# Kernel tuning notes

Measured on AMD Instinct MI355X. Metric: run time of the kernel, lower is better.

Reference implementation:

```python
import jax, jax.numpy as jnp
import numpy as np

K_TOP = 2  # n_experts_per_tok
W_SCALE = 0.02  # keep activations numerically tame


def setup_inputs() -> dict:
    key = jax.random.key(0)
    ks = jax.random.split(key, 8)
    D, F, E = 1024, 1024, 8
    B, T = 4, 2048
    x = jax.random.normal(ks[0], (B, T, D), dtype=jnp.float32)
    router_w = jax.random.normal(ks[1], (D, E), dtype=jnp.float32) * W_SCALE
    sg = jax.random.normal(ks[2], (D, F), dtype=jnp.float32) * W_SCALE
    su = jax.random.normal(ks[3], (D, F), dtype=jnp.float32) * W_SCALE
    sd = jax.random.normal(ks[4], (F, D), dtype=jnp.float32) * W_SCALE
    wg = jax.random.normal(ks[5], (E, D, F), dtype=jnp.float32) * W_SCALE
    wu = jax.random.normal(ks[6], (E, D, F), dtype=jnp.float32) * W_SCALE
    wd = jax.random.normal(ks[7], (E, F, D), dtype=jnp.float32) * W_SCALE
    return {"x": x, "router_w": router_w, "sg": sg, "su": su, "sd": sd,
            "wg": wg, "wu": wu, "wd": wd}


def reference(x, router_w, sg, su, sd, wg, wu, wd):
    B, T, D = x.shape
    E = wg.shape[0]
    flat = x.reshape(-1, D)                       # [N, D]
    N = flat.shape[0]

    # shared SwiGLU expert (n_shared_experts = 1)
    shared = (jax.nn.silu(flat @ sg) * (flat @ su)) @ sd  # [N, D]

    # top-k softmax router with renormalization
    probs = jax.nn.softmax(flat @ router_w, axis=-1)      # [N, E]
    topk_p, topk_i = jax.lax.top_k(probs, K_TOP)          # [N, K]
    topk_p = topk_p / (jnp.sum(topk_p, axis=-1, keepdims=True) + 1e-9)

    # dense combine weights: scatter renormalized probs into [N, E]
    cw = jnp.zeros((N, E), dtype=flat.dtype).at[
        jnp.arange(N)[:, None], topk_i].add(topk_p)

    # per-expert SwiGLU on all tokens, weighted combine (jit-friendly MoE form)
    h = jax.nn.silu(jnp.einsum('nd,edf->nef', flat, wg)) \
        * jnp.einsum('nd,edf->nef', flat, wu)             # [N, E, F]
    eo = jnp.einsum('nef,efd->ned', h, wd)                # [N, E, D]
    routed = jnp.einsum('ned,ne->nd', eo, cw)             # [N, D]

    return (shared + routed).reshape(B, T, D)
```

## Files before the change

### kernel.cpp

```cpp
#include <hip/hip_runtime.h>

#define N_TOK    8192
#define D_DIM    1024
#define F_DIM    1024
#define NESH     9
#define MAX_RTD  18432
#define MAX_ROWS 26624
#define BM 256
#define BN 128
#define BK 64
#define BN2 256

#define MO 16
#define MT 25

typedef float  f4    __attribute__((ext_vector_type(4)));
typedef float  f32x4 __attribute__((ext_vector_type(4)));
typedef short  s16x8 __attribute__((ext_vector_type(8)));
typedef unsigned short u16x8 __attribute__((ext_vector_type(8)));

static __device__ __forceinline__ unsigned short f2bf(float f) {
    union { float f; unsigned u; } v; v.f = f;
    unsigned r = v.u + 0x7FFFu + ((v.u >> 16) & 1u);
    return (unsigned short)(r >> 16);
}
static __device__ __forceinline__ float bf2f(unsigned short u) {
    union { unsigned u; float f; } v; v.u = ((unsigned)u) << 16; return v.f;
}

#define GLDS(gp, lp) __builtin_amdgcn_global_load_lds( \
    (const __attribute__((address_space(1))) void*)(gp), \
    (__attribute__((address_space(3))) void*)(lp), 16, 0, 0)

#define RSWZ(row, idx) ((idx) ^ (((row) & 7) << 3))

__global__ __launch_bounds__(256) void k_convert_x(
    const float* __restrict__ x, unsigned short* __restrict__ xb)
{
    int g = blockIdx.x * 256 + threadIdx.x;
    const f4* xs = (const f4*)x;
    f4 a = xs[2*g], b = xs[2*g+1];
    u16x8 o;
    o[0]=f2bf(a[0]); o[1]=f2bf(a[1]); o[2]=f2bf(a[2]); o[3]=f2bf(a[3]);
    o[4]=f2bf(b[0]); o[5]=f2bf(b[1]); o[6]=f2bf(b[2]); o[7]=f2bf(b[3]);
    *(u16x8*)&xb[8*(size_t)g] = o;
}

__global__ __launch_bounds__(256) void k_transpose(
    const float* __restrict__ wg, const float* __restrict__ wu,
    const float* __restrict__ wd, const float* __restrict__ sg,
    const float* __restrict__ su, const float* __restrict__ sd,
    unsigned short* __restrict__ wgt, unsigned short* __restrict__ wut,
    unsigned short* __restrict__ wdt)
{
    int bx = blockIdx.x;
    int m = bx >> 8;
    int tile = bx & 255;
    int ty = tile >> 4, tx = tile & 15;
    int set = m / 9, e = m % 9;
    const float* src; unsigned short* dst;
    if (set == 0)      { src = (e < 8) ? wg + (size_t)e*1048576 : sg; dst = wgt + (size_t)e*1048576; }
    else if (set == 1) { src = (e < 8) ? wu + (size_t)e*1048576 : su; dst = wut + (size_t)e*1048576; }
    else               { src = (e < 8) ? wd + (size_t)e*1048576 : sd; dst = wdt + (size_t)e*1048576; }

    __shared__ __align__(16) unsigned short ts[64 * 80];
    int t = threadIdx.x;
    int rT0 = ty * 64, cT0 = tx * 64;
    #pragma unroll
    for (int i = 0; i < 16; i++) {
        int lin = t + i * 256;
        int mr = lin >> 6, mc = lin & 63;
        float v = src[(size_t)(cT0 + mr) * 1024 + rT0 + mc];
        ts[mc * 80 + mr] = f2bf(v);
    }
    __syncthreads();
    #pragma unroll
    for (int i = 0; i < 2; i++) {
        int r = (t >> 3) + i * 32;
        int c0 = (t & 7) * 8;
        *(u16x8*)&dst[(size_t)(rT0 + r) * 1024 + cT0 + c0] = *(u16x8*)&ts[r * 80 + c0];
    }
}

__global__ __launch_bounds__(256) void k_router(
    const float* __restrict__ x, const float* __restrict__ rw,
    int* __restrict__ tk_i, float* __restrict__ tk_w)
{
    int wid = threadIdx.x >> 6, lane = threadIdx.x & 63;
    int n = blockIdx.x * 4 + wid;
    const float* xr = x + (size_t)n * D_DIM;
    float acc[8] = {0,0,0,0,0,0,0,0};
    #pragma unroll
    for (int it = 0; it < 16; it++) {
        int d = it * 64 + lane;
        float xv = xr[d];
        f4 r0 = *(const f4*)(rw + (size_t)d * 8);
        f4 r1 = *(const f4*)(rw + (size_t)d * 8 + 4);
        acc[0] += xv * r0[0]; acc[1] += xv * r0[1]; acc[2] += xv * r0[2]; acc[3] += xv * r0[3];
        acc[4] += xv * r1[0]; acc[5] += xv * r1[1]; acc[6] += xv * r1[2]; acc[7] += xv * r1[3];
    }
    #pragma unroll
    for (int e = 0; e < 8; e++)
        for (int off = 32; off; off >>= 1)
            acc[e] += __shfl_xor(acc[e], off, 64);
    if (lane == 0) {
        float mx = acc[0];
        for (int e = 1; e < 8; e++) mx = fmaxf(mx, acc[e]);
        float p[8], s = 0.f;
        for (int e = 0; e < 8; e++) { p[e] = expf(acc[e] - mx); s += p[e]; }
        int i0 = 0;
        for (int e = 1; e < 8; e++) if (p[e] > p[i0]) i0 = e;
        int i1 = (i0 == 0) ? 1 : 0;
        for (int e = 0; e < 8; e++) if (e != i0 && p[e] > p[i1]) i1 = e;
        float p0 = p[i0] / s, p1 = p[i1] / s;
        float rs = p0 + p1 + 1e-9f;
        tk_i[2*n] = i0;  tk_i[2*n+1] = i1;
        tk_w[2*n] = p0 / rs;  tk_w[2*n+1] = p1 / rs;
    }
}

__global__ __launch_bounds__(256) void k_prefill(int* __restrict__ row_token)
{
    int i = blockIdx.x * 256 + threadIdx.x;
    row_token[i] = -1;
}

__global__ __launch_bounds__(1024) void k_count_scatter(
    const int* __restrict__ tk_i, const float* __restrict__ tk_w,
    int* __restrict__ meta,
    int* __restrict__ row_token, int* __restrict__ row_expert,
    int* __restrict__ tok_pos)
{
    __shared__ int cnt[1024 * 9];
    __shared__ int tot[8];
    __shared__ int off[9];
    const int t = threadIdx.x;
    const int lane = t & 63;
    const int wid = t >> 6;

    #pragma unroll
    for (int e = 0; e < 8; e++) cnt[t * 9 + e] = 0;
    __syncthreads();

    #pragma unroll
    for (int j = 0; j < 8; j++) {
        int n = t * 8 + j;
        cnt[t * 9 + tk_i[2 * n]]++;
        cnt[t * 9 + tk_i[2 * n + 1]]++;
    }
    __syncthreads();

    if (wid < 8) {
        const int e = wid;
        int carry = 0;
        for (int c = 0; c < 16; c++) {
            int i = c * 64 + lane;
            int v = cnt[i * 9 + e];
            int s = v;
            #pragma unroll
// ... 6 lines not shown
        }
        if (lane == 0) tot[e] = carry;
    }
    __syncthreads();

    if (t == 0) {
        int acc = 0;
        #pragma unroll
        for (int e = 0; e < 8; e++) {
            off[e] = acc;
            meta[MO + e] = acc;
            acc += ((tot[e] + 255) >> 8) << 8;
        }
        off[8] = acc;
        meta[MO + 8] = acc;
        meta[MT] = acc + N_TOK;
    }
    __syncthreads();

    #pragma unroll
    for (int j = 0; j < 8; j++) {
        int n = t * 8 + j;
        #pragma unroll
        for (int k = 0; k < 2; k++) {
            int e = tk_i[2 * n + k];
            int pos = off[e] + cnt[t * 9 + e];
            cnt[t * 9 + e] = cnt[t * 9 + e] + 1;
            row_token[pos] = n; row_expert[pos] = e;
            tok_pos[2 * n + k] = pos;
        }
        int ps = off[8] + n;
        row_token[ps] = n; row_expert[ps] = 8;
    }
}

__global__ __launch_bounds__(512, 2) void k_gemm1(
    const unsigned short* __restrict__ xb,
    const unsigned short* __restrict__ wgt,
    const unsigned short* __restrict__ wut,
    const int* __restrict__ row_token,
    const int* __restrict__ row_expert,
    const int* __restrict__ meta,
    unsigned short* __restrict__ h)
{
    const int total = meta[MT];
    const int orig = blockIdx.x;
    const int bid = (orig & 7) * 104 + (orig >> 3);
    const int rt = bid >> 3, ct = bid & 7;
    const int row0 = rt * BM;
    if (row0 >= total) return;
    const int e = row_expert[row0];

    __shared__ __align__(16) unsigned short sA[2 * BM * BK];
    __shared__ __align__(16) unsigned short sBg[2 * BN * BK];
    __shared__ __align__(16) unsigned short sBu[2 * BN * BK];

    const int t = threadIdx.x;
    const int lane = t & 63;
    const int wid = t >> 6;
    const int wr = wid >> 1, wc = wid & 1;

    const unsigned short* asrc[4];
    #pragma unroll
    for (int i = 0; i < 4; i++) {
        int slot = t + i * 512;
        int row = slot >> 3;
        int cg  = (slot & 7) ^ (row & 7);
        int tok = row_token[row0 + row];
        if (tok < 0) tok = 0;
        asrc[i] = xb + (size_t)tok * D_DIM + cg * 8;
    }
    const unsigned short* bsrcg[2];
    const unsigned short* bsrcu[2];
    #pragma unroll
    for (int i = 0; i < 2; i++) {
        int slot = t + i * 512;
        int row = slot >> 3;
        int cg  = (slot & 7) ^ (row & 7);
        size_t off = ((size_t)e * F_DIM + ct * BN + row) * D_DIM + cg * 8;
        bsrcg[i] = wgt + off;
        bsrcu[i] = wut + off;
    }

    f32x4 accg[4][4] = {}, accu[4][4] = {};

#define STAGE1(bb, k0) do { \
    unsigned short* dA  = &sA[(bb) * (BM * BK)]; \
    unsigned short* dBg = &sBg[(bb) * (BN * BK)]; \
    unsigned short* dBu = &sBu[(bb) * (BN * BK)]; \
    _Pragma("unroll") \
    for (int i_ = 0; i_ < 4; i_++) GLDS(asrc[i_] + (k0), &dA[(t + i_ * 512) * 8]); \
    _Pragma("unroll") \
    for (int i_ = 0; i_ < 2; i_++) { \
        GLDS(bsrcg[i_] + (k0), &dBg[(t + i_ * 512) * 8]); \
        GLDS(bsrcu[i_] + (k0), &dBu[(t + i_ * 512) * 8]); \
    } } while (0)

#define COMPUTE1(bb) do { \
    const unsigned short* pA  = &sA[(bb) * (BM * BK)]; \
    const unsigned short* pBg = &sBg[(bb) * (BN * BK)]; \
    const unsigned short* pBu = &sBu[(bb) * (BN * BK)]; \
    _Pragma("unroll") \
    for (int kk = 0; kk < BK; kk += 32) { \
        const int koff = kk + (lane >> 4) * 8; \
        s16x8 a_[4], bg_[4], bu_[4]; \
        _Pragma("unroll") \
        for (int m_ = 0; m_ < 4; m_++) { \
            int row = wr * 64 + m_ * 16 + (lane & 15); \
            a_[m_] = *(const s16x8*)&pA[RSWZ(row, row * BK + koff)]; } \
        _Pragma("unroll") \
        for (int n_ = 0; n_ < 4; n_++) { \
            int row = wc * 64 + n_ * 16 + (lane & 15); \
            bg_[n_] = *(const s16x8*)&pBg[RSWZ(row, row * BK + koff)]; \
            bu_[n_] = *(const s16x8*)&pBu[RSWZ(row, row * BK + koff)]; } \
        _Pragma("unroll") \
        for (int m_ = 0; m_ < 4; m_++) \
            _Pragma("unroll") \
            for (int n_ = 0; n_ < 4; n_++) { \
                accg[m_][n_] = __builtin_amdgcn_mfma_f32_16x16x32_bf16(a_[m_], bg_[n_], accg[m_][n_], 0, 0, 0); \
                accu[m_][n_] = __builtin_amdgcn_mfma_f32_16x16x32_bf16(a_[m_], bu_[n_], accu[m_][n_], 0, 0, 0); } \
    } } while (0)

    STAGE1(0, 0);
    int cur = 0;
    for (int k0 = 0; k0 < D_DIM - BK; k0 += BK) {
        STAGE1(cur ^ 1, k0 + BK);
        asm volatile("s_waitcnt vmcnt(8)" ::: "memory");
        __builtin_amdgcn_s_barrier();
        __builtin_amdgcn_s_setprio(1);
        COMPUTE1(cur);
        __builtin_amdgcn_s_setprio(0);
        asm volatile("" ::: "memory");
        __builtin_amdgcn_s_barrier();
        cur ^= 1;
    }
    asm volatile("s_waitcnt vmcnt(0)" ::: "memory");
    __builtin_amdgcn_s_barrier();
    __builtin_amdgcn_s_setprio(1);
    COMPUTE1(cur);
    __builtin_amdgcn_s_setprio(0);

    #pragma unroll
    for (int m = 0; m < 4; m++)
        #pragma unroll
        for (int r = 0; r < 4; r++) {
            int grow = row0 + wr * 64 + m * 16 + (lane >> 4) * 4 + r;
            unsigned short* hrow = h + (size_t)grow * F_DIM + ct * BN + wc * 64 + (lane & 15);
            #pragma unroll
            for (int n = 0; n < 4; n++) {
                float g = accg[m][n][r], u = accu[m][n][r];
                float sv = g / (1.f + __expf(-g));
                hrow[n * 16] = f2bf(sv * u);
            }
        }
#undef STAGE1
#undef COMPUTE1
}

__global__ __launch_bounds__(512, 2) void k_gemm2(
    const unsigned short* __restrict__ h,
    const unsigned short* __restrict__ wdt,
    const int* __restrict__ row_expert,
    const int* __restrict__ meta,
    unsigned short* __restrict__ eo,
    float* __restrict__ out)
{
    const int total = meta[MT];
    const int off8 = meta[MO + 8];
    const int orig = blockIdx.x;
    const int bid = (orig & 7) * 52 + (orig >> 3);
    const int rt = bid >> 2, ct = bid & 3;
    const int row0 = rt * BM;
    if (row0 >= total) return;
    const int e = row_expert[row0];

    __shared__ __align__(16) unsigned short sA[2 * BM * BK];
    __shared__ __align__(16) unsigned short sB[2 * BN2 * BK];

    const int t = threadIdx.x;
    const int lane = t & 63;
    const int wid = t >> 6;
    const int wr = wid >> 2, wc = wid & 3;

    const unsigned short* asrc[4];
    #pragma unroll
    for (int i = 0; i < 4; i++) {
        int slot = t + i * 512;
        int row = slot >> 3;
        int cg  = (slot & 7) ^ (row & 7);
        asrc[i] = h + (size_t)(row0 + row) * F_DIM + cg * 8;
    }
    const unsigned short* bsrc[4];
    #pragma unroll
    for (int i = 0; i < 4; i++) {
        int slot = t + i * 512;
        int row = slot >> 3;
        int cg  = (slot & 7) ^ (row & 7);
        bsrc[i] = wdt + ((size_t)e * D_DIM + ct * BN2 + row) * F_DIM + cg * 8;
    }

    f32x4 acc[8][4] = {};

#define STAGE2(bb, k0) do { \
    unsigned short* dA = &sA[(bb) * (BM * BK)]; \
    unsigned short* dB = &sB[(bb) * (BN2 * BK)]; \
    _Pragma("unroll") \
    for (int i_ = 0; i_ < 4; i_++) GLDS(asrc[i_] + (k0), &dA[(t + i_ * 512) * 8]); \
    _Pragma("unroll") \
    for (int i_ = 0; i_ < 4; i_++) GLDS(bsrc[i_] + (k0), &dB[(t + i_ * 512) * 8]); \
    } while (0)

#define COMPUTE2(bb) do { \
    const unsigned short* pA = &sA[(bb) * (BM * BK)]; \
    const unsigned short* pB = &sB[(bb) * (BN2 * BK)]; \
    _Pragma("unroll") \
    for (int kk = 0; kk < BK; kk += 32) { \
        const int koff = kk + (lane >> 4) * 8; \
        s16x8 a_[8], b_[4]; \
        _Pragma("unroll") \
        for (int m_ = 0; m_ < 8; m_++) { \
            int row = wr * 128 + m_ * 16 + (lane & 15); \
            a_[m_] = *(const s16x8*)&pA[RSWZ(row, row * BK + koff)]; } \
        _Pragma("unroll") \
        for (int n_ = 0; n_ < 4; n_++) { \
            int row = wc * 64 + n_ * 16 + (lane & 15); \
            b_[n_] = *(const s16x8*)&pB[RSWZ(row, row * BK + koff)]; } \
        _Pragma("unroll") \
        for (int m_ = 0; m_ < 8; m_++) \
            _Pragma("unroll") \
            for (int n_ = 0; n_ < 4; n_++) \
                acc[m_][n_] = __builtin_amdgcn_mfma_f32_16x16x32_bf16(a_[m_], b_[n_], acc[m_][n_], 0, 0, 0); \
    } } while (0)

    STAGE2(0, 0);
    int cur = 0;
    for (int k0 = 0; k0 < F_DIM - BK; k0 += BK) {
        STAGE2(cur ^ 1, k0 + BK);
        asm volatile("s_waitcnt vmcnt(8)" ::: "memory");
        __builtin_amdgcn_s_barrier();
        __builtin_amdgcn_s_setprio(1);
        COMPUTE2(cur);
        __builtin_amdgcn_s_setprio(0);
        asm volatile("" ::: "memory");
        __builtin_amdgcn_s_barrier();
        cur ^= 1;
    }
    asm volatile("s_waitcnt vmcnt(0)" ::: "memory");
    __builtin_amdgcn_s_barrier();
    __builtin_amdgcn_s_setprio(1);
    COMPUTE2(cur);
    __builtin_amdgcn_s_setprio(0);

    if (e < 8) {
        #pragma unroll
        for (int m = 0; m < 8; m++)
            #pragma unroll
            for (int r = 0; r < 4; r++) {
                int grow = row0 + wr * 128 + m * 16 + (lane >> 4) * 4 + r;
                unsigned short* erow = eo + (size_t)grow * D_DIM + ct * BN2 + wc * 64 + (lane & 15);
                #pragma unroll
                for (int n = 0; n < 4; n++)
                    erow[n * 16] = f2bf(acc[m][n][r]);
            }
    } else {
        #pragma unroll
        for (int m = 0; m < 8; m++)
            #pragma unroll
            for (int r = 0; r < 4; r++) {
                int grow = row0 + wr * 128 + m * 16 + (lane >> 4) * 4 + r;
                int tok = grow - off8;
                float* orow = out + (size_t)tok * D_DIM + ct * BN2 + wc * 64 + (lane & 15);
                #pragma unroll
                for (int n = 0; n < 4; n++)
                    orow[n * 16] = acc[m][n][r];
            }
    }
#undef STAGE2
#undef COMPUTE2
}

__global__ __launch_bounds__(256) void k_combine(
    const unsigned short* __restrict__ eo,
    const int* __restrict__ tok_pos, const float* __restrict__ tk_w,
    float* __restrict__ out)
{
    const int t = threadIdx.x;
    const int n = blockIdx.x * 2 + (t >> 7);
    const int c0 = (t & 127) * 8;
    const int p0 = tok_pos[2 * n], p1 = tok_pos[2 * n + 1];
    const float w0 = tk_w[2 * n], w1 = tk_w[2 * n + 1];
    u16x8 a = *(const u16x8*)&eo[(size_t)p0 * D_DIM + c0];
    u16x8 b = *(const u16x8*)&eo[(size_t)p1 * D_DIM + c0];
    float* orow = out + (size_t)n * D_DIM + c0;
    f4 o0 = *(f4*)orow, o1 = *(f4*)(orow + 4);
    #pragma unroll
    for (int j = 0; j < 4; j++) {
        o0[j] += w0 * bf2f(a[j])     + w1 * bf2f(b[j]);
        o1[j] += w0 * bf2f(a[4 + j]) + w1 * bf2f(b[4 + j]);
    }
    *(f4*)orow = o0;
    *(f4*)(orow + 4) = o1;
}

extern "C" void kernel_launch(void* const* d_in, const int* in_sizes, int n_in,
                              void* d_out, int out_size, void* d_ws, size_t ws_size,
                              hipStream_t stream)
{
    const float* x  = (const float*)d_in[0];
    const float* rw = (const float*)d_in[1];
    const float* sg = (const float*)d_in[2];
    const float* su = (const float*)d_in[3];
    const float* sd = (const float*)d_in[4];
    const float* wg = (const float*)d_in[5];
    const float* wu = (const float*)d_in[6];
    const float* wd = (const float*)d_in[7];
    float* out = (float*)d_out;

    char* p = (char*)d_ws;
    unsigned short* xb  = (unsigned short*)p; p += (size_t)N_TOK * D_DIM * 2;
    unsigned short* wgt = (unsigned short*)p; p += (size_t)NESH * D_DIM * F_DIM * 2;
    unsigned short* wut = (unsigned short*)p; p += (size_t)NESH * D_DIM * F_DIM * 2;
    unsigned short* wdt = (unsigned short*)p; p += (size_t)NESH * D_DIM * F_DIM * 2;
    unsigned short* h   = (unsigned short*)p; p += (size_t)MAX_ROWS * F_DIM * 2;
    int*   row_token  = (int*)p;   p += (size_t)MAX_ROWS * 4;
    int*   row_expert = (int*)p;   p += (size_t)MAX_ROWS * 4;
    int*   tok_pos = (int*)p;      p += (size_t)N_TOK * 2 * 4;
    int*   tk_i = (int*)p;         p += (size_t)N_TOK * 2 * 4;
    float* tk_w = (float*)p;       p += (size_t)N_TOK * 2 * 4;
    int*   meta = (int*)p;         p += 1024;
    if ((size_t)(p - (char*)d_ws) > ws_size) return;

    unsigned short* eo = wgt;

    k_convert_x<<<N_TOK * D_DIM / 8 / 256, 256, 0, stream>>>(x, xb);
    k_transpose<<<27 * 256, 256, 0, stream>>>(wg, wu, wd, sg, su, sd, wgt, wut, wdt);
    k_router<<<N_TOK / 4, 256, 0, stream>>>(x, rw, tk_i, tk_w);
    k_prefill<<<MAX_ROWS / 256, 256, 0, stream>>>(row_token);
    k_count_scatter<<<1, 1024, 0, stream>>>(tk_i, tk_w, meta, row_token, row_expert, tok_pos);
    k_gemm1<<<(MAX_ROWS / BM) * 8, 512, 0, stream>>>(xb, wgt, wut, row_token, row_expert, meta, h);
    k_gemm2<<<(MAX_ROWS / BM) * 4, 512, 0, stream>>>(h, wdt, row_expert, meta, eo, out);
    k_combine<<<N_TOK / 2, 256, 0, stream>>>(eo, tok_pos, tk_w, out);
}
```

Before: 306.8 us.

## Rework GEMM pipelines to 4-slot BK32 schedule and fuse preprocessing kernels

Both grouped GEMMs switch from double-buffered BK=64 stages to a four-slot BK=32 ring. Loads are interleaved across four compute phases per iteration so global-to-LDS copies overlap MFMA work, and GEMM1 uses a new 2x4 wave layout. The x-to-bf16 conversion is fused into the router kernel, and row_token padding is written only for the padded tail rows inside count_scatter instead of by a separate prefill kernel. The weight transpose now uses vectorized float4 reads with an odd-stride LDS tile. These changes cut launches and memory passes but make the hand-written vmcnt/barrier pipeline more fragile.

Result: slower. 354.7 us (+15.6%).

```diff
diff --git a/kernel.cpp b/kernel.cpp
--- a/kernel.cpp
+++ b/kernel.cpp
@@ -7,9 +7,7 @@
 #define MAX_RTD  18432
 #define MAX_ROWS 26624
 #define BM 256
-#define BN 128
-#define BK 64
-#define BN2 256
+#define NK 16
 
 #define MO 16
 #define MT 25
@@ -18,6 +16,7 @@
 typedef float  f32x4 __attribute__((ext_vector_type(4)));
 typedef short  s16x8 __attribute__((ext_vector_type(8)));
 typedef unsigned short u16x8 __attribute__((ext_vector_type(8)));
+typedef unsigned short u16x4 __attribute__((ext_vector_type(4)));
 
 static __device__ __forceinline__ unsigned short f2bf(float f) {
     union { float f; unsigned u; } v; v.f = f;
@@ -31,20 +30,6 @@
 #define GLDS(gp, lp) __builtin_amdgcn_global_load_lds( \
     (const __attribute__((address_space(1))) void*)(gp), \
     (__attribute__((address_space(3))) void*)(lp), 16, 0, 0)
-
-#define RSWZ(row, idx) ((idx) ^ (((row) & 7) << 3))
-
-__global__ __launch_bounds__(256) void k_convert_x(
-    const float* __restrict__ x, unsigned short* __restrict__ xb)
-{
-    int g = blockIdx.x * 256 + threadIdx.x;
-    const f4* xs = (const f4*)x;
-    f4 a = xs[2*g], b = xs[2*g+1];
-    u16x8 o;
-    o[0]=f2bf(a[0]); o[1]=f2bf(a[1]); o[2]=f2bf(a[2]); o[3]=f2bf(a[3]);
-    o[4]=f2bf(b[0]); o[5]=f2bf(b[1]); o[6]=f2bf(b[2]); o[7]=f2bf(b[3]);
-    *(u16x8*)&xb[8*(size_t)g] = o;
-}
 
 __global__ __launch_bounds__(256) void k_transpose(
     const float* __restrict__ wg, const float* __restrict__ wu,
@@ -63,41 +48,56 @@
     else if (set == 1) { src = (e < 8) ? wu + (size_t)e*1048576 : su; dst = wut + (size_t)e*1048576; }
     else               { src = (e < 8) ? wd + (size_t)e*1048576 : sd; dst = wdt + (size_t)e*1048576; }
 
-    __shared__ __align__(16) unsigned short ts[64 * 80];
+    __shared__ unsigned short ts[64 * 67];
     int t = threadIdx.x;
     int rT0 = ty * 64, cT0 = tx * 64;
     #pragma unroll
-    for (int i = 0; i < 16; i++) {
-        int lin = t + i * 256;
-        int mr = lin >> 6, mc = lin & 63;
-        float v = src[(size_t)(cT0 + mr) * 1024 + rT0 + mc];
-        ts[mc * 80 + mr] = f2bf(v);
+    for (int i = 0; i < 4; i++) {
+        int idx = t + i * 256;
+        int a  = idx >> 4;
+        int b4 = (idx & 15) * 4;
+        f4 v = *(const f4*)(src + (size_t)(cT0 + a) * 1024 + rT0 + b4);
+        ts[a * 67 + b4 + 0] = f2bf(v[0]);
+        ts[a * 67 + b4 + 1] = f2bf(v[1]);
+        ts[a * 67 + b4 + 2] = f2bf(v[2]);
+        ts[a * 67 + b4 + 3] = f2bf(v[3]);
     }
     __syncthreads();
     #pragma unroll
     for (int i = 0; i < 2; i++) {
-        int r = (t >> 3) + i * 32;
-        int c0 = (t & 7) * 8;
-        *(u16x8*)&dst[(size_t)(rT0 + r) * 1024 + cT0 + c0] = *(u16x8*)&ts[r * 80 + c0];
+        int slot = t + i * 256;
+        int r  = slot >> 3;
+        int c8 = (slot & 7) * 8;
+        u16x8 o;
+        #pragma unroll
+        for (int k = 0; k < 8; k++) o[k] = ts[(c8 + k) * 67 + r];
+        *(u16x8*)&dst[(size_t)(rT0 + r) * 1024 + cT0 + c8] = o;
     }
 }
 
 __global__ __launch_bounds__(256) void k_router(
     const float* __restrict__ x, const float* __restrict__ rw,
+    unsigned short* __restrict__ xb,
     int* __restrict__ tk_i, float* __restrict__ tk_w)
 {
     int wid = threadIdx.x >> 6, lane = threadIdx.x & 63;
     int n = blockIdx.x * 4 + wid;
     const float* xr = x + (size_t)n * D_DIM;
+    unsigned short* xbr = xb + (size_t)n * D_DIM;
     float acc[8] = {0,0,0,0,0,0,0,0};
     #pragma unroll
-    for (int it = 0; it < 16; it++) {
-        int d = it * 64 + lane;
-        float xv = xr[d];
-        f4 r0 = *(const f4*)(rw + (size_t)d * 8);
-        f4 r1 = *(const f4*)(rw + (size_t)d * 8 + 4);
-        acc[0] += xv * r0[0]; acc[1] += xv * r0[1]; acc[2] += xv * r0[2]; acc[3] += xv * r0[3];
-        acc[4] += xv * r1[0]; acc[5] += xv * r1[1]; acc[6] += xv * r1[2]; acc[7] += xv * r1[3];
+    for (int it = 0; it < 4; it++) {
+        int d0 = it * 256 + lane * 4;
+        f4 xv = *(const f4*)(xr + d0);
+        #pragma unroll
+        for (int j = 0; j < 4; j++) {
+            f4 r0 = *(const f4*)(rw + (size_t)(d0 + j) * 8);
+            f4 r1 = *(const f4*)(rw + (size_t)(d0 + j) * 8 + 4);
+            acc[0] += xv[j]*r0[0]; acc[1] += xv[j]*r0[1]; acc[2] += xv[j]*r0[2]; acc[3] += xv[j]*r0[3];
+            acc[4] += xv[j]*r1[0]; acc[5] += xv[j]*r1[1]; acc[6] += xv[j]*r1[2]; acc[7] += xv[j]*r1[3];
+        }
+        u16x4 o; o[0]=f2bf(xv[0]); o[1]=f2bf(xv[1]); o[2]=f2bf(xv[2]); o[3]=f2bf(xv[3]);
+        *(u16x4*)&xbr[d0] = o;
     }
     #pragma unroll
     for (int e = 0; e < 8; e++)
@@ -119,12 +119,6 @@
     }
 }
 
-__global__ __launch_bounds__(256) void k_prefill(int* __restrict__ row_token)
-{
-    int i = blockIdx.x * 256 + threadIdx.x;
-    row_token[i] = -1;
-}
-
 __global__ __launch_bounds__(1024) void k_count_scatter(
     const int* __restrict__ tk_i, const float* __restrict__ tk_w,
     int* __restrict__ meta,
@@ -197,6 +191,11 @@
         int ps = off[8] + n;
         row_token[ps] = n; row_expert[ps] = 8;
     }
+    #pragma unroll
+    for (int e = 0; e < 8; e++) {
+        int start = off[e] + tot[e], end = off[e + 1];
+        for (int i = start + t; i < end; i += 1024) row_token[i] = -1;
+    }
 }
 
 __global__ __launch_bounds__(512, 2) void k_gemm1(
@@ -216,110 +215,103 @@
     if (row0 >= total) return;
     const int e = row_expert[row0];
 
-    __shared__ __align__(16) unsigned short sA[2 * BM * BK];
-    __shared__ __align__(16) unsigned short sBg[2 * BN * BK];
-    __shared__ __align__(16) unsigned short sBu[2 * BN * BK];
+    __shared__ __align__(16) unsigned short sA[4 * 256 * 32];
+    __shared__ __align__(16) unsigned short sBg[4 * 128 * 32];
+    __shared__ __align__(16) unsigned short sBu[4 * 128 * 32];
 
     const int t = threadIdx.x;
     const int lane = t & 63;
+    const int klane = lane >> 4;
     const int wid = t >> 6;
-    const int wr = wid >> 1, wc = wid & 1;
-
-    const unsigned short* asrc[4];
-    #pragma unroll
-    for (int i = 0; i < 4; i++) {
-        int slot = t + i * 512;
-        int row = slot >> 3;
-        int cg  = (slot & 7) ^ (row & 7);
+    const int wr = wid >> 2, wc = wid & 3;
+
+    const unsigned short* aA[2];
+    #pragma unroll
+    for (int r = 0; r < 2; r++) {
+        int slot = t + r * 512;
+        int row = slot >> 2;
+        int cg = (slot & 3) ^ ((row >> 1) & 3);
         int tok = row_token[row0 + row];
         if (tok < 0) tok = 0;
-        asrc[i] = xb + (size_t)tok * D_DIM + cg * 8;
-    }
-    const unsigned short* bsrcg[2];
-    const unsigned short* bsrcu[2];
-    #pragma unroll
-    for (int i = 0; i < 2; i++) {
-        int slot = t + i * 512;
-        int row = slot >> 3;
-        int cg  = (slot & 7) ^ (row & 7);
-        size_t off = ((size_t)e * F_DIM + ct * BN + row) * D_DIM + cg * 8;
-        bsrcg[i] = wgt + off;
-        bsrcu[i] = wut + off;
-    }
-
-    f32x4 accg[4][4] = {}, accu[4][4] = {};
-
-#define STAGE1(bb, k0) do { \
-    unsigned short* dA  = &sA[(bb) * (BM * BK)]; \
-    unsigned short* dBg = &sBg[(bb) * (BN * BK)]; \
-    unsigned short* dBu = &sBu[(bb) * (BN * BK)]; \
-    _Pragma("unroll") \
-    for (int i_ = 0; i_ < 4; i_++) GLDS(asrc[i_] + (k0), &dA[(t + i_ * 512) * 8]); \
-    _Pragma("unroll") \
-    for (int i_ = 0; i_ < 2; i_++) { \
-        GLDS(bsrcg[i_] + (k0), &dBg[(t + i_ * 512) * 8]); \
-        GLDS(bsrcu[i_] + (k0), &dBu[(t + i_ * 512) * 8]); \
-    } } while (0)
-
-#define COMPUTE1(bb) do { \
-    const unsigned short* pA  = &sA[(bb) * (BM * BK)]; \
-    const unsigned short* pBg = &sBg[(bb) * (BN * BK)]; \
-    const unsigned short* pBu = &sBu[(bb) * (BN * BK)]; \
-    _Pragma("unroll") \
-    for (int kk = 0; kk < BK; kk += 32) { \
-        const int koff = kk + (lane >> 4) * 8; \
-        s16x8 a_[4], bg_[4], bu_[4]; \
+        aA[r] = xb + (size_t)tok * D_DIM + cg * 8;
+    }
+    const int brow = t >> 2;
+    const int bcg = (t & 3) ^ ((brow >> 1) & 3);
+    const unsigned short* bG = wgt + ((size_t)e * F_DIM + ct * 128 + brow) * D_DIM + bcg * 8;
+    const unsigned short* bU = wut + ((size_t)e * F_DIM + ct * 128 + brow) * D_DIM + bcg * 8;
+
+#define ST_A(sl, ko) do { \
+    GLDS(aA[0] + (ko), &sA[(sl) * 8192 + t * 8]); \
+    GLDS(aA[1] + (ko), &sA[(sl) * 8192 + (t + 512) * 8]); } while (0)
+#define ST_G(sl, ko) GLDS(bG + (ko), &sBg[(sl) * 4096 + t * 8])
+#define ST_U(sl, ko) GLDS(bU + (ko), &sBu[(sl) * 4096 + t * 8])
+
+#define G1_PHASE(bb, ss, hh, STAGE_STMT, VM_STMT) do { \
+    const unsigned short* pA = &sA[((bb)*2 + (ss)) * 8192]; \
+    const unsigned short* pG = &sBg[((bb)*2 + (ss)) * 4096]; \
+    const unsigned short* pU = &sBu[((bb)*2 + (ss)) * 4096]; \
+    s16x8 a_[4], g_[2], q_[2]; \
+    _Pragma("unroll") \
+    for (int mi = 0; mi < 4; mi++) { \
+        int row = wr * 128 + (hh) * 64 + mi * 16 + (lane & 15); \
+        a_[mi] = *(const s16x8*)&pA[row * 32 + ((klane ^ ((row >> 1) & 3)) << 3)]; } \
+    _Pragma("unroll") \
+    for (int ni = 0; ni < 2; ni++) { \
+        int row = wc * 32 + ni * 16 + (lane & 15); \
+        int ix = row * 32 + ((klane ^ ((row >> 1) & 3)) << 3); \
+        g_[ni] = *(const s16x8*)&pG[ix]; \
+        q_[ni] = *(const s16x8*)&pU[ix]; } \
+    STAGE_STMT; \
+    VM_STMT; \
+    asm volatile("s_barrier" ::: "memory"); \
+    __builtin_amdgcn_s_setprio(1); \
+    _Pragma("unroll") \
+    for (int mi = 0; mi < 4; mi++) \
         _Pragma("unroll") \
-        for (int m_ = 0; m_ < 4; m_++) { \
-            int row = wr * 64 + m_ * 16 + (lane & 15); \
-            a_[m_] = *(const s16x8*)&pA[RSWZ(row, row * BK + koff)]; } \
-        _Pragma("unroll") \
-        for (int n_ = 0; n_ < 4; n_++) { \
-            int row = wc * 64 + n_ * 16 + (lane & 15); \
-            bg_[n_] = *(const s16x8*)&pBg[RSWZ(row, row * BK + koff)]; \
-            bu_[n_] = *(const s16x8*)&pBu[RSWZ(row, row * BK + koff)]; } \
-        _Pragma("unroll") \
-        for (int m_ = 0; m_ < 4; m_++) \
-            _Pragma("unroll") \
-            for (int n_ = 0; n_ < 4; n_++) { \
-                accg[m_][n_] = __builtin_amdgcn_mfma_f32_16x16x32_bf16(a_[m_], bg_[n_], accg[m_][n_], 0, 0, 0); \
-                accu[m_][n_] = __builtin_amdgcn_mfma_f32_16x16x32_bf16(a_[m_], bu_[n_], accu[m_][n_], 0, 0, 0); } \
-    } } while (0)
-
-    STAGE1(0, 0);
-    int cur = 0;
-    for (int k0 = 0; k0 < D_DIM - BK; k0 += BK) {
-        STAGE1(cur ^ 1, k0 + BK);
-        asm volatile("s_waitcnt vmcnt(8)" ::: "memory");
-        __builtin_amdgcn_s_barrier();
-        __builtin_amdgcn_s_setprio(1);
-        COMPUTE1(cur);
-        __builtin_amdgcn_s_setprio(0);
-        asm volatile("" ::: "memory");
-        __builtin_amdgcn_s_barrier();
-        cur ^= 1;
-    }
-    asm volatile("s_waitcnt vmcnt(0)" ::: "memory");
-    __builtin_amdgcn_s_barrier();
-    __builtin_amdgcn_s_setprio(1);
-    COMPUTE1(cur);
-    __builtin_amdgcn_s_setprio(0);
-
-    #pragma unroll
-    for (int m = 0; m < 4; m++)
+        for (int ni = 0; ni < 2; ni++) { \
+            accg[(hh)*4+mi][ni] = __builtin_amdgcn_mfma_f32_16x16x32_bf16(a_[mi], g_[ni], accg[(hh)*4+mi][ni], 0, 0, 0); \
+            accu[(hh)*4+mi][ni] = __builtin_amdgcn_mfma_f32_16x16x32_bf16(a_[mi], q_[ni], accu[(hh)*4+mi][ni], 0, 0, 0); } \
+    __builtin_amdgcn_s_setprio(0); \
+    asm volatile("s_barrier" ::: "memory"); \
+} while (0)
+
+    f32x4 accg[8][2] = {}, accu[8][2] = {};
+
+    ST_A(0, 0);  ST_G(0, 0);  ST_U(0, 0);
+    ST_A(1, 32); ST_G(1, 32); ST_U(1, 32);
+    ST_A(2, 64); ST_G(2, 64); ST_U(2, 64);
+    ST_A(3, 96);
+    asm volatile("s_waitcnt vmcnt(6)" ::: "memory");
+    asm volatile("s_barrier" ::: "memory");
+
+    for (int u = 0; u < NK; u++) {
+        const int b = u & 1, nb = b ^ 1;
+        const int o1 = (u + 1) * 64 + 32, o2 = (u + 2) * 64;
+        G1_PHASE(b, 0, 0, if (u < NK-1) { ST_G(nb*2+1, o1); ST_U(nb*2+1, o1); }, );
+        G1_PHASE(b, 0, 1, if (u < NK-2) { ST_A(b*2, o2); }, );
+        G1_PHASE(b, 1, 0, if (u < NK-2) { ST_G(b*2, o2); ST_U(b*2, o2); }, );
+        G1_PHASE(b, 1, 1, if (u < NK-2) { ST_A(b*2+1, o2+32); },
+                 if (u < NK-2) { asm volatile("s_waitcnt vmcnt(6)" ::: "memory"); }
+                 else if (u == NK-2) { asm volatile("s_waitcnt vmcnt(0)" ::: "memory"); });
+    }
+
+    #pragma unroll
+    for (int mf = 0; mf < 8; mf++)
         #pragma unroll
         for (int r = 0; r < 4; r++) {
-            int grow = row0 + wr * 64 + m * 16 + (lane >> 4) * 4 + r;
-            unsigned short* hrow = h + (size_t)grow * F_DIM + ct * BN + wc * 64 + (lane & 15);
+            int grow = row0 + wr * 128 + mf * 16 + (lane >> 4) * 4 + r;
+            unsigned short* hrow = h + (size_t)grow * F_DIM + ct * 128 + wc * 32 + (lane & 15);
             #pragma unroll
-            for (int n = 0; n < 4; n++) {
-                float g = accg[m][n][r], u = accu[m][n][r];
+            for (int ni = 0; ni < 2; ni++) {
+                float g = accg[mf][ni][r], uu = accu[mf][ni][r];
                 float sv = g / (1.f + __expf(-g));
-                hrow[n * 16] = f2bf(sv * u);
+                hrow[ni * 16] = f2bf(sv * uu);
             }
         }
-#undef STAGE1
-#undef COMPUTE1
+#undef ST_A
+#undef ST_G
+#undef ST_U
+#undef G1_PHASE
 }
 
 __global__ __launch_bounds__(512, 2) void k_gemm2(
@@ -339,109 +331,105 @@
     if (row0 >= total) return;
     const int e = row_expert[row0];
 
-    __shared__ __align__(16) unsigned short sA[2 * BM * BK];
-    __shared__ __align__(16) unsigned short sB[2 * BN2 * BK];
+    __shared__ __align__(16) unsigned short sA[4 * 256 * 32];
+    __shared__ __align__(16) unsigned short sB[4 * 256 * 32];
 
     const int t = threadIdx.x;
     const int lane = t & 63;
+    const int klane = lane >> 4;
     const int wid = t >> 6;
     const int wr = wid >> 2, wc = wid & 3;
 
-    const unsigned short* asrc[4];
-    #pragma unroll
-    for (int i = 0; i < 4; i++) {
-        int slot = t + i * 512;
-        int row = slot >> 3;
-        int cg  = (slot & 7) ^ (row & 7);
-        asrc[i] = h + (size_t)(row0 + row) * F_DIM + cg * 8;
-    }
-    const unsigned short* bsrc[4];
-    #pragma unroll
-    for (int i = 0; i < 4; i++) {
-        int slot = t + i * 512;
-        int row = slot >> 3;
-        int cg  = (slot & 7) ^ (row & 7);
-        bsrc[i] = wdt + ((size_t)e * D_DIM + ct * BN2 + row) * F_DIM + cg * 8;
-    }
+    const unsigned short* aA[2];
+    const unsigned short* bB[2];
+    #pragma unroll
+    for (int r = 0; r < 2; r++) {
+        int slot = t + r * 512;
+        int row = slot >> 2;
+        int cg = (slot & 3) ^ ((row >> 1) & 3);
+        aA[r] = h + (size_t)(row0 + row) * F_DIM + cg * 8;
+        bB[r] = wdt + ((size_t)e * D_DIM + ct * 256 + row) * F_DIM + cg * 8;
+    }
+
+#define ST_A2(sl, ko) do { \
+    GLDS(aA[0] + (ko), &sA[(sl) * 8192 + t * 8]); \
+    GLDS(aA[1] + (ko), &sA[(sl) * 8192 + (t + 512) * 8]); } while (0)
+#define ST_B2(sl, ko) do { \
+    GLDS(bB[0] + (ko), &sB[(sl) * 8192 + t * 8]); \
+    GLDS(bB[1] + (ko), &sB[(sl) * 8192 + (t + 512) * 8]); } while (0)
+
+#define G2_PHASE(bb, ss, hh, STAGE_STMT, VM_STMT) do { \
+    const unsigned short* pA = &sA[((bb)*2 + (ss)) * 8192]; \
+    const unsigned short* pB = &sB[((bb)*2 + (ss)) * 8192]; \
+    s16x8 a_[4], b_[4]; \
+    _Pragma("unroll") \
+    for (int mi = 0; mi < 4; mi++) { \
+        int row = wr * 128 + (hh) * 64 + mi * 16 + (lane & 15); \
+        a_[mi] = *(const s16x8*)&pA[row * 32 + ((klane ^ ((row >> 1) & 3)) << 3)]; } \
+    _Pragma("unroll") \
+    for (int ni = 0; ni < 4; ni++) { \
+        int row = wc * 64 + ni * 16 + (lane & 15); \
+        b_[ni] = *(const s16x8*)&pB[row * 32 + ((klane ^ ((row >> 1) & 3)) << 3)]; } \
+    STAGE_STMT; \
+    VM_STMT; \
+    asm volatile("s_barrier" ::: "memory"); \
+    __builtin_amdgcn_s_setprio(1); \
+    _Pragma("unroll") \
+    for (int mi = 0; mi < 4; mi++) \
+        _Pragma("unroll") \
+        for (int ni = 0; ni < 4; ni++) \
+            acc[(hh)*4+mi][ni] = __builtin_amdgcn_mfma_f32_16x16x32_bf16(a_[mi], b_[ni], acc[(hh)*4+mi][ni], 0, 0, 0); \
+    __builtin_amdgcn_s_setprio(0); \
+    asm volatile("s_barrier" ::: "memory"); \
+} while (0)
 
     f32x4 acc[8][4] = {};
 
-#define STAGE2(bb, k0) do { \
-    unsigned short* dA = &sA[(bb) * (BM * BK)]; \
-    unsigned short* dB = &sB[(bb) * (BN2 * BK)]; \
-    _Pragma("unroll") \
-    for (int i_ = 0; i_ < 4; i_++) GLDS(asrc[i_] + (k0), &dA[(t + i_ * 512) * 8]); \
-    _Pragma("unroll") \
-    for (int i_ = 0; i_ < 4; i_++) GLDS(bsrc[i_] + (k0), &dB[(t + i_ * 512) * 8]); \
-    } while (0)
-
-#define COMPUTE2(bb) do { \
-    const unsigned short* pA = &sA[(bb) * (BM * BK)]; \
-    const unsigned short* pB = &sB[(bb) * (BN2 * BK)]; \
-    _Pragma("unroll") \
-    for (int kk = 0; kk < BK; kk += 32) { \
-        const int koff = kk + (lane >> 4) * 8; \
-        s16x8 a_[8], b_[4]; \
-        _Pragma("unroll") \
-        for (int m_ = 0; m_ < 8; m_++) { \
-            int row = wr * 128 + m_ * 16 + (lane & 15); \
-            a_[m_] = *(const s16x8*)&pA[RSWZ(row, row * BK + koff)]; } \
-        _Pragma("unroll") \
-        for (int n_ = 0; n_ < 4; n_++) { \
-            int row = wc * 64 + n_ * 16 + (lane & 15); \
-            b_[n_] = *(const s16x8*)&pB[RSWZ(row, row * BK + koff)]; } \
-        _Pragma("unroll") \
-        for (int m_ = 0; m_ < 8; m_++) \
-            _Pragma("unroll") \
-            for (int n_ = 0; n_ < 4; n_++) \
-                acc[m_][n_] = __builtin_amdgcn_mfma_f32_16x16x32_bf16(a_[m_], b_[n_], acc[m_][n_], 0, 0, 0); \
-    } } while (0)
-
-    STAGE2(0, 0);
-    int cur = 0;
-    for (int k0 = 0; k0 < F_DIM - BK; k0 += BK) {
-        STAGE2(cur ^ 1, k0 + BK);
-        asm volatile("s_waitcnt vmcnt(8)" ::: "memory");
-        __builtin_amdgcn_s_barrier();
-        __builtin_amdgcn_s_setprio(1);
-        COMPUTE2(cur);
-        __builtin_amdgcn_s_setprio(0);
-        asm volatile("" ::: "memory");
-        __builtin_amdgcn_s_barrier();
-        cur ^= 1;
-    }
-    asm volatile("s_waitcnt vmcnt(0)" ::: "memory");
-    __builtin_amdgcn_s_barrier();
-    __builtin_amdgcn_s_setprio(1);
-    COMPUTE2(cur);
-    __builtin_amdgcn_s_setprio(0);
+    ST_A2(0, 0);  ST_B2(0, 0);
+    ST_A2(1, 32); ST_B2(1, 32);
+    ST_A2(2, 64); ST_B2(2, 64);
+    ST_A2(3, 96);
+    asm volatile("s_waitcnt vmcnt(6)" ::: "memory");
+    asm volatile("s_barrier" ::: "memory");
+
+    for (int u = 0; u < NK; u++) {
+        const int b = u & 1, nb = b ^ 1;
+        const int o1 = (u + 1) * 64 + 32, o2 = (u + 2) * 64;
+        G2_PHASE(b, 0, 0, if (u < NK-1) { ST_B2(nb*2+1, o1); }, );
+        G2_PHASE(b, 0, 1, if (u < NK-2) { ST_A2(b*2, o2); }, );
+        G2_PHASE(b, 1, 0, if (u < NK-2) { ST_B2(b*2, o2); }, );
+        G2_PHASE(b, 1, 1, if (u < NK-2) { ST_A2(b*2+1, o2+32); },
+                 if (u < NK-2) { asm volatile("s_waitcnt vmcnt(6)" ::: "memory"); }
+                 else if (u == NK-2) { asm volatile("s_waitcnt vmcnt(0)" ::: "memory"); });
+    }
 
     if (e < 8) {
         #pragma unroll
-        for (int m = 0; m < 8; m++)
+        for (int mf = 0; mf < 8; mf++)
             #pragma unroll
             for (int r = 0; r < 4; r++) {
-                int grow = row0 + wr * 128 + m * 16 + (lane >> 4) * 4 + r;
-                unsigned short* erow = eo + (size_t)grow * D_DIM + ct * BN2 + wc * 64 + (lane & 15);
+                int grow = row0 + wr * 128 + mf * 16 + (lane >> 4) * 4 + r;
+                unsigned short* erow = eo + (size_t)grow * D_DIM + ct * 256 + wc * 64 + (lane & 15);
                 #pragma unroll
-                for (int n = 0; n < 4; n++)
-                    erow[n * 16] = f2bf(acc[m][n][r]);
+                for (int ni = 0; ni < 4; ni++)
+                    erow[ni * 16] = f2bf(acc[mf][ni][r]);
             }
     } else {
         #pragma unroll
-        for (int m = 0; m < 8; m++)
+        for (int mf = 0; mf < 8; mf++)
             #pragma unroll
             for (int r = 0; r < 4; r++) {
-                int grow = row0 + wr * 128 + m * 16 + (lane >> 4) * 4 + r;
+                int grow = row0 + wr * 128 + mf * 16 + (lane >> 4) * 4 + r;
                 int tok = grow - off8;
-                float* orow = out + (size_t)tok * D_DIM + ct * BN2 + wc * 64 + (lane & 15);
+                float* orow = out + (size_t)tok * D_DIM + ct * 256 + wc * 64 + (lane & 15);
                 #pragma unroll
-                for (int n = 0; n < 4; n++)
-                    orow[n * 16] = acc[m][n][r];
+                for (int ni = 0; ni < 4; ni++)
+                    orow[ni * 16] = acc[mf][ni][r];
             }
     }
-#undef STAGE2
-#undef COMPUTE2
+#undef ST_A2
+#undef ST_B2
+#undef G2_PHASE
 }
 
 __global__ __launch_bounds__(256) void k_combine(
@@ -497,10 +485,8 @@
 
     unsigned short* eo = wgt;
 
-    k_convert_x<<<N_TOK * D_DIM / 8 / 256, 256, 0, stream>>>(x, xb);
+    k_router<<<N_TOK / 4, 256, 0, stream>>>(x, rw, xb, tk_i, tk_w);
     k_transpose<<<27 * 256, 256, 0, stream>>>(wg, wu, wd, sg, su, sd, wgt, wut, wdt);
-    k_router<<<N_TOK / 4, 256, 0, stream>>>(x, rw, tk_i, tk_w);
-    k_prefill<<<MAX_ROWS / 256, 256, 0, stream>>>(row_token);
     k_count_scatter<<<1, 1024, 0, stream>>>(tk_i, tk_w, meta, row_token, row_expert, tok_pos);
     k_gemm1<<<(MAX_ROWS / BM) * 8, 512, 0, stream>>>(xb, wgt, wut, row_token, row_expert, meta, h);
     k_gemm2<<<(MAX_ROWS / BM) * 4, 512, 0, stream>>>(h, wdt, row_expert, meta, eo, out);
```

## Fuse x conversion into router, drop prefill, triple-buffer B tiles in GEMMs

Applied to the files above, without the earlier changes.

Folds the fp32-to-bf16 conversion of x into the router kernel and removes the separate prefill kernel by padding row_token inside count_scatter, cutting two launches and one full pass over x. The transpose kernel now reads weights with vectorized f4 loads and uses a padded LDS tile. Both grouped GEMMs move to a 3-stage ring buffer for the weight (B) tiles with deeper vmcnt waits, keeping A double-buffered, to hide more global latency. The extra LDS may reduce occupancy at launch bound 2, and the waitcnt counts must match the issued loads exactly.

After: 323.5 us. +5.5%, slower.

```diff
diff --git a/kernel.cpp b/kernel.cpp
--- a/kernel.cpp
+++ b/kernel.cpp
@@ -7,9 +7,8 @@
 #define MAX_RTD  18432
 #define MAX_ROWS 26624
 #define BM 256
-#define BN 128
 #define BK 64
-#define BN2 256
+#define NK 16
 
 #define MO 16
 #define MT 25
@@ -18,6 +17,7 @@
 typedef float  f32x4 __attribute__((ext_vector_type(4)));
 typedef short  s16x8 __attribute__((ext_vector_type(8)));
 typedef unsigned short u16x8 __attribute__((ext_vector_type(8)));
+typedef unsigned short u16x4 __attribute__((ext_vector_type(4)));
 
 static __device__ __forceinline__ unsigned short f2bf(float f) {
     union { float f; unsigned u; } v; v.f = f;
@@ -33,18 +33,6 @@
     (__attribute__((address_space(3))) void*)(lp), 16, 0, 0)
 
 #define RSWZ(row, idx) ((idx) ^ (((row) & 7) << 3))
-
-__global__ __launch_bounds__(256) void k_convert_x(
-    const float* __restrict__ x, unsigned short* __restrict__ xb)
-{
-    int g = blockIdx.x * 256 + threadIdx.x;
-    const f4* xs = (const f4*)x;
-    f4 a = xs[2*g], b = xs[2*g+1];
-    u16x8 o;
-    o[0]=f2bf(a[0]); o[1]=f2bf(a[1]); o[2]=f2bf(a[2]); o[3]=f2bf(a[3]);
-    o[4]=f2bf(b[0]); o[5]=f2bf(b[1]); o[6]=f2bf(b[2]); o[7]=f2bf(b[3]);
-    *(u16x8*)&xb[8*(size_t)g] = o;
-}
 
 __global__ __launch_bounds__(256) void k_transpose(
     const float* __restrict__ wg, const float* __restrict__ wu,
@@ -63,41 +51,56 @@
     else if (set == 1) { src = (e < 8) ? wu + (size_t)e*1048576 : su; dst = wut + (size_t)e*1048576; }
     else               { src = (e < 8) ? wd + (size_t)e*1048576 : sd; dst = wdt + (size_t)e*1048576; }
 
-    __shared__ __align__(16) unsigned short ts[64 * 80];
+    __shared__ unsigned short ts[64 * 67];
     int t = threadIdx.x;
     int rT0 = ty * 64, cT0 = tx * 64;
     #pragma unroll
-    for (int i = 0; i < 16; i++) {
-        int lin = t + i * 256;
-        int mr = lin >> 6, mc = lin & 63;
-        float v = src[(size_t)(cT0 + mr) * 1024 + rT0 + mc];
-        ts[mc * 80 + mr] = f2bf(v);
+    for (int i = 0; i < 4; i++) {
+        int idx = t + i * 256;
+        int a  = idx >> 4;
+        int b4 = (idx & 15) * 4;
+        f4 v = *(const f4*)(src + (size_t)(cT0 + a) * 1024 + rT0 + b4);
+        ts[a * 67 + b4 + 0] = f2bf(v[0]);
+        ts[a * 67 + b4 + 1] = f2bf(v[1]);
+        ts[a * 67 + b4 + 2] = f2bf(v[2]);
+        ts[a * 67 + b4 + 3] = f2bf(v[3]);
     }
     __syncthreads();
     #pragma unroll
     for (int i = 0; i < 2; i++) {
-        int r = (t >> 3) + i * 32;
-        int c0 = (t & 7) * 8;
-        *(u16x8*)&dst[(size_t)(rT0 + r) * 1024 + cT0 + c0] = *(u16x8*)&ts[r * 80 + c0];
+        int slot = t + i * 256;
+        int r  = slot >> 3;
+        int c8 = (slot & 7) * 8;
+        u16x8 o;
+        #pragma unroll
+        for (int k = 0; k < 8; k++) o[k] = ts[(c8 + k) * 67 + r];
+        *(u16x8*)&dst[(size_t)(rT0 + r) * 1024 + cT0 + c8] = o;
     }
 }
 
 __global__ __launch_bounds__(256) void k_router(
     const float* __restrict__ x, const float* __restrict__ rw,
+    unsigned short* __restrict__ xb,
     int* __restrict__ tk_i, float* __restrict__ tk_w)
 {
     int wid = threadIdx.x >> 6, lane = threadIdx.x & 63;
     int n = blockIdx.x * 4 + wid;
     const float* xr = x + (size_t)n * D_DIM;
+    unsigned short* xbr = xb + (size_t)n * D_DIM;
     float acc[8] = {0,0,0,0,0,0,0,0};
     #pragma unroll
-    for (int it = 0; it < 16; it++) {
-        int d = it * 64 + lane;
-        float xv = xr[d];
-        f4 r0 = *(const f4*)(rw + (size_t)d * 8);
-        f4 r1 = *(const f4*)(rw + (size_t)d * 8 + 4);
-        acc[0] += xv * r0[0]; acc[1] += xv * r0[1]; acc[2] += xv * r0[2]; acc[3] += xv * r0[3];
-        acc[4] += xv * r1[0]; acc[5] += xv * r1[1]; acc[6] += xv * r1[2]; acc[7] += xv * r1[3];
+    for (int it = 0; it < 4; it++) {
+        int d0 = it * 256 + lane * 4;
+        f4 xv = *(const f4*)(xr + d0);
+        #pragma unroll
+        for (int j = 0; j < 4; j++) {
+            f4 r0 = *(const f4*)(rw + (size_t)(d0 + j) * 8);
+            f4 r1 = *(const f4*)(rw + (size_t)(d0 + j) * 8 + 4);
+            acc[0] += xv[j]*r0[0]; acc[1] += xv[j]*r0[1]; acc[2] += xv[j]*r0[2]; acc[3] += xv[j]*r0[3];
+            acc[4] += xv[j]*r1[0]; acc[5] += xv[j]*r1[1]; acc[6] += xv[j]*r1[2]; acc[7] += xv[j]*r1[3];
+        }
+        u16x4 o; o[0]=f2bf(xv[0]); o[1]=f2bf(xv[1]); o[2]=f2bf(xv[2]); o[3]=f2bf(xv[3]);
+        *(u16x4*)&xbr[d0] = o;
     }
     #pragma unroll
     for (int e = 0; e < 8; e++)
@@ -119,12 +122,6 @@
     }
 }
 
-__global__ __launch_bounds__(256) void k_prefill(int* __restrict__ row_token)
-{
-    int i = blockIdx.x * 256 + threadIdx.x;
-    row_token[i] = -1;
-}
-
 __global__ __launch_bounds__(1024) void k_count_scatter(
     const int* __restrict__ tk_i, const float* __restrict__ tk_w,
     int* __restrict__ meta,
@@ -197,6 +194,11 @@
         int ps = off[8] + n;
         row_token[ps] = n; row_expert[ps] = 8;
     }
+    #pragma unroll
+    for (int e = 0; e < 8; e++) {
+        int start = off[e] + tot[e], end = off[e + 1];
+        for (int i = start + t; i < end; i += 1024) row_token[i] = -1;
+    }
 }
 
 __global__ __launch_bounds__(512, 2) void k_gemm1(
@@ -217,8 +219,8 @@
     const int e = row_expert[row0];
 
     __shared__ __align__(16) unsigned short sA[2 * BM * BK];
-    __shared__ __align__(16) unsigned short sBg[2 * BN * BK];
-    __shared__ __align__(16) unsigned short sBu[2 * BN * BK];
+    __shared__ __align__(16) unsigned short sBg[3 * 128 * BK];
+    __shared__ __align__(16) unsigned short sBu[3 * 128 * BK];
 
     const int t = threadIdx.x;
     const int lane = t & 63;
@@ -242,29 +244,31 @@
         int slot = t + i * 512;
         int row = slot >> 3;
         int cg  = (slot & 7) ^ (row & 7);
-        size_t off = ((size_t)e * F_DIM + ct * BN + row) * D_DIM + cg * 8;
+        size_t off = ((size_t)e * F_DIM + ct * 128 + row) * D_DIM + cg * 8;
         bsrcg[i] = wgt + off;
         bsrcu[i] = wut + off;
     }
 
     f32x4 accg[4][4] = {}, accu[4][4] = {};
 
-#define STAGE1(bb, k0) do { \
-    unsigned short* dA  = &sA[(bb) * (BM * BK)]; \
-    unsigned short* dBg = &sBg[(bb) * (BN * BK)]; \
-    unsigned short* dBu = &sBu[(bb) * (BN * BK)]; \
+#define STAGE_A1(bb, k0) do { \
+    unsigned short* dA = &sA[(bb) * (BM * BK)]; \
     _Pragma("unroll") \
     for (int i_ = 0; i_ < 4; i_++) GLDS(asrc[i_] + (k0), &dA[(t + i_ * 512) * 8]); \
+    } while (0)
+#define STAGE_B1(ss, k0) do { \
+    unsigned short* dBg = &sBg[(ss) * (128 * BK)]; \
+    unsigned short* dBu = &sBu[(ss) * (128 * BK)]; \
     _Pragma("unroll") \
     for (int i_ = 0; i_ < 2; i_++) { \
         GLDS(bsrcg[i_] + (k0), &dBg[(t + i_ * 512) * 8]); \
         GLDS(bsrcu[i_] + (k0), &dBu[(t + i_ * 512) * 8]); \
     } } while (0)
 
-#define COMPUTE1(bb) do { \
+#define COMPUTE1(bb, ss) do { \
     const unsigned short* pA  = &sA[(bb) * (BM * BK)]; \
-    const unsigned short* pBg = &sBg[(bb) * (BN * BK)]; \
-    const unsigned short* pBu = &sBu[(bb) * (BN * BK)]; \
+    const unsigned short* pBg = &sBg[(ss) * (128 * BK)]; \
+    const unsigned short* pBu = &sBu[(ss) * (128 * BK)]; \
     _Pragma("unroll") \
     for (int kk = 0; kk < BK; kk += 32) { \
         const int koff = kk + (lane >> 4) * 8; \
@@ -286,31 +290,38 @@
                 accu[m_][n_] = __builtin_amdgcn_mfma_f32_16x16x32_bf16(a_[m_], bu_[n_], accu[m_][n_], 0, 0, 0); } \
     } } while (0)
 
-    STAGE1(0, 0);
-    int cur = 0;
-    for (int k0 = 0; k0 < D_DIM - BK; k0 += BK) {
-        STAGE1(cur ^ 1, k0 + BK);
-        asm volatile("s_waitcnt vmcnt(8)" ::: "memory");
+    STAGE_A1(0, 0);
+    STAGE_B1(0, 0);
+    STAGE_B1(1, BK);
+
+    int sc = 0;
+    int sst = 2;
+    for (int u = 0; u < NK; u++) {
+        if (u < NK - 1) STAGE_A1((u + 1) & 1, (u + 1) * BK);
+        if (u < NK - 2) {
+            STAGE_B1(sst, (u + 2) * BK);
+            asm volatile("s_waitcnt vmcnt(12)" ::: "memory");
+        } else if (u < NK - 1) {
+            asm volatile("s_waitcnt vmcnt(8)" ::: "memory");
+        } else {
+            asm volatile("s_waitcnt vmcnt(0)" ::: "memory");
+        }
         __builtin_amdgcn_s_barrier();
         __builtin_amdgcn_s_setprio(1);
-        COMPUTE1(cur);
+        COMPUTE1(u & 1, sc);
         __builtin_amdgcn_s_setprio(0);
         asm volatile("" ::: "memory");
         __builtin_amdgcn_s_barrier();
-        cur ^= 1;
-    }
-    asm volatile("s_waitcnt vmcnt(0)" ::: "memory");
-    __builtin_amdgcn_s_barrier();
-    __builtin_amdgcn_s_setprio(1);
-    COMPUTE1(cur);
-    __builtin_amdgcn_s_setprio(0);
+        sc  = (sc  == 2) ? 0 : sc + 1;
+        sst = (sst == 2) ? 0 : sst + 1;
+    }
 
     #pragma unroll
     for (int m = 0; m < 4; m++)
         #pragma unroll
         for (int r = 0; r < 4; r++) {
             int grow = row0 + wr * 64 + m * 16 + (lane >> 4) * 4 + r;
-            unsigned short* hrow = h + (size_t)grow * F_DIM + ct * BN + wc * 64 + (lane & 15);
+            unsigned short* hrow = h + (size_t)grow * F_DIM + ct * 128 + wc * 64 + (lane & 15);
             #pragma unroll
             for (int n = 0; n < 4; n++) {
                 float g = accg[m][n][r], u = accu[m][n][r];
@@ -318,7 +329,8 @@
                 hrow[n * 16] = f2bf(sv * u);
             }
         }
-#undef STAGE1
+#undef STAGE_A1
+#undef STAGE_B1
 #undef COMPUTE1
 }
 
@@ -340,7 +352,7 @@
     const int e = row_expert[row0];
 
     __shared__ __align__(16) unsigned short sA[2 * BM * BK];
-    __shared__ __align__(16) unsigned short sB[2 * BN2 * BK];
+    __shared__ __align__(16) unsigned short sB[3 * 256 * BK];
 
     const int t = threadIdx.x;
     const int lane = t & 63;
@@ -348,36 +360,32 @@
     const int wr = wid >> 2, wc = wid & 3;
 
     const unsigned short* asrc[4];
+    const unsigned short* bsrc[4];
     #pragma unroll
     for (int i = 0; i < 4; i++) {
         int slot = t + i * 512;
         int row = slot >> 3;
         int cg  = (slot & 7) ^ (row & 7);
         asrc[i] = h + (size_t)(row0 + row) * F_DIM + cg * 8;
-    }
-    const unsigned short* bsrc[4];
-    #pragma unroll
-    for (int i = 0; i < 4; i++) {
-        int slot = t + i * 512;
-        int row = slot >> 3;
-        int cg  = (slot & 7) ^ (row & 7);
-        bsrc[i] = wdt + ((size_t)e * D_DIM + ct * BN2 + row) * F_DIM + cg * 8;
+        bsrc[i] = wdt + ((size_t)e * D_DIM + ct * 256 + row) * F_DIM + cg * 8;
     }
 
     f32x4 acc[8][4] = {};
 
-#define STAGE2(bb, k0) do { \
+#define STAGE_A2(bb, k0) do { \
     unsigned short* dA = &sA[(bb) * (BM * BK)]; \
-    unsigned short* dB = &sB[(bb) * (BN2 * BK)]; \
     _Pragma("unroll") \
     for (int i_ = 0; i_ < 4; i_++) GLDS(asrc[i_] + (k0), &dA[(t + i_ * 512) * 8]); \
+    } while (0)
+#define STAGE_B2(ss, k0) do { \
+    unsigned short* dB = &sB[(ss) * (256 * BK)]; \
     _Pragma("unroll") \
     for (int i_ = 0; i_ < 4; i_++) GLDS(bsrc[i_] + (k0), &dB[(t + i_ * 512) * 8]); \
     } while (0)
 
-#define COMPUTE2(bb) do { \
+#define COMPUTE2(bb, ss) do { \
     const unsigned short* pA = &sA[(bb) * (BM * BK)]; \
-    const unsigned short* pB = &sB[(bb) * (BN2 * BK)]; \
+    const unsigned short* pB = &sB[(ss) * (256 * BK)]; \
     _Pragma("unroll") \
     for (int kk = 0; kk < BK; kk += 32) { \
         const int koff = kk + (lane >> 4) * 8; \
@@ -397,50 +405,57 @@
                 acc[m_][n_] = __builtin_amdgcn_mfma_f32_16x16x32_bf16(a_[m_], b_[n_], acc[m_][n_], 0, 0, 0); \
     } } while (0)
 
-    STAGE2(0, 0);
-    int cur = 0;
-    for (int k0 = 0; k0 < F_DIM - BK; k0 += BK) {
-        STAGE2(cur ^ 1, k0 + BK);
-        asm volatile("s_waitcnt vmcnt(8)" ::: "memory");
+    STAGE_A2(0, 0);
+    STAGE_B2(0, 0);
+    STAGE_B2(1, BK);
+
+    int sc = 0, sst = 2;
+    for (int u = 0; u < NK; u++) {
+        if (u < NK - 1) STAGE_A2((u + 1) & 1, (u + 1) * BK);
+        if (u < NK - 2) {
+            STAGE_B2(sst, (u + 2) * BK);
+            asm volatile("s_waitcnt vmcnt(12)" ::: "memory");
+        } else if (u < NK - 1) {
+            asm volatile("s_waitcnt vmcnt(8)" ::: "memory");
+        } else {
+            asm volatile("s_waitcnt vmcnt(0)" ::: "memory");
+        }
         __builtin_amdgcn_s_barrier();
         __builtin_amdgcn_s_setprio(1);
-        COMPUTE2(cur);
+        COMPUTE2(u & 1, sc);
         __builtin_amdgcn_s_setprio(0);
         asm volatile("" ::: "memory");
         __builtin_amdgcn_s_barrier();
-        cur ^= 1;
-    }
-    asm volatile("s_waitcnt vmcnt(0)" ::: "memory");
-    __builtin_amdgcn_s_barrier();
-    __builtin_amdgcn_s_setprio(1);
-    COMPUTE2(cur);
-    __builtin_amdgcn_s_setprio(0);
+        sc  = (sc  == 2) ? 0 : sc + 1;
+        sst = (sst == 2) ? 0 : sst + 1;
+    }
 
     if (e < 8) {
         #pragma unroll
-        for (int m = 0; m < 8; m++)
+        for (int mf = 0; mf < 8; mf++)
             #pragma unroll
             for (int r = 0; r < 4; r++) {
-                int grow = row0 + wr * 128 + m * 16 + (lane >> 4) * 4 + r;
-                unsigned short* erow = eo + (size_t)grow * D_DIM + ct * BN2 + wc * 64 + (lane & 15);
+                int grow = row0 + wr * 128 + mf * 16 + (lane >> 4) * 4 + r;
+                unsigned short* erow = eo + (size_t)grow * D_DIM + ct * 256 + wc * 64 + (lane & 15);
                 #pragma unroll
-                for (int n = 0; n < 4; n++)
-                    erow[n * 16] = f2bf(acc[m][n][r]);
+                for (int ni = 0; ni < 4; ni++)
+                    erow[ni * 16] = f2bf(acc[mf][ni][r]);
             }
     } else {
         #pragma unroll
-        for (int m = 0; m < 8; m++)
+        for (int mf = 0; mf < 8; mf++)
             #pragma unroll
             for (int r = 0; r < 4; r++) {
-                int grow = row0 + wr * 128 + m * 16 + (lane >> 4) * 4 + r;
+                int grow = row0 + wr * 128 + mf * 16 + (lane >> 4) * 4 + r;
                 int tok = grow - off8;
-                float* orow = out + (size_t)tok * D_DIM + ct * BN2 + wc * 64 + (lane & 15);
+                float* orow = out + (size_t)tok * D_DIM + ct * 256 + wc * 64 + (lane & 15);
                 #pragma unroll
-                for (int n = 0; n < 4; n++)
-                    orow[n * 16] = acc[m][n][r];
+                for (int ni = 0; ni < 4; ni++)
+                    orow[ni * 16] = acc[mf][ni][r];
             }
     }
-#undef STAGE2
+#undef STAGE_A2
+#undef STAGE_B2
 #undef COMPUTE2
 }
 
@@ -497,10 +512,8 @@
 
     unsigned short* eo = wgt;
 
-    k_convert_x<<<N_TOK * D_DIM / 8 / 256, 256, 0, stream>>>(x, xb);
+    k_router<<<N_TOK / 4, 256, 0, stream>>>(x, rw, xb, tk_i, tk_w);
     k_transpose<<<27 * 256, 256, 0, stream>>>(wg, wu, wd, sg, su, sd, wgt, wut, wdt);
-    k_router<<<N_TOK / 4, 256, 0, stream>>>(x, rw, tk_i, tk_w);
-    k_prefill<<<MAX_ROWS / 256, 256, 0, stream>>>(row_token);
     k_count_scatter<<<1, 1024, 0, stream>>>(tk_i, tk_w, meta, row_token, row_expert, tok_pos);
     k_gemm1<<<(MAX_ROWS / BM) * 8, 512, 0, stream>>>(xb, wgt, wut, row_token, row_expert, meta, h);
     k_gemm2<<<(MAX_ROWS / BM) * 4, 512, 0, stream>>>(h, wdt, row_expert, meta, eo, out);
```
